# Performance work log

Hardware: AMD Instinct MI355X
Metric: run time of the kernel (lower is better)

## Reference

```python
import jax, jax.numpy as jnp
import numpy as np

N, E, D, H = 20000, 320000, 128, 256
N_ITER = 3

def _w(k, fi, fo):
    return jax.random.normal(k, (fi, fo), jnp.float32) / np.sqrt(fi)

def setup_inputs() -> dict:
    key = jax.random.key(0)
    ks = jax.random.split(key, 16)
    inp = {
        "x": jax.random.normal(ks[0], (N, D), jnp.float32),
        "edge_attr": jax.random.normal(ks[1], (E, D), jnp.float32),
        "edge_index": jax.random.randint(ks[2], (2, E), 0, N, jnp.int32),
        # EASP edge encoder: cat[src,tgt,edge] (3D) -> H -> D
        "enc_w1": _w(ks[3], 3 * D, H), "enc_b1": jnp.zeros((H,), jnp.float32),
        "enc_w2": _w(ks[4], H, D), "enc_b2": jnp.zeros((D,), jnp.float32),
        # EdgeCNN: cat[src(2D), tgt(2D), edge(2D)] = 6D -> H -> D (reattach doubles dims)
        "em_w1": _w(ks[5], 6 * D, H), "em_b1": jnp.zeros((H,), jnp.float32),
        "em_w2": _w(ks[6], H, D), "em_b2": jnp.zeros((D,), jnp.float32),
        # node message MLP: cat[x_src(2D), edge(D)] = 3D -> H -> D
        "nm_w1": _w(ks[7], 3 * D, H), "nm_b1": jnp.zeros((H,), jnp.float32),
        "nm_w2": _w(ks[8], H, D), "nm_b2": jnp.zeros((D,), jnp.float32),
        # node output linear after aggregation
        "no_w": _w(ks[9], D, D), "no_b": jnp.zeros((D,), jnp.float32),
        # shared LayerNorms (ModuleList([layer]*n_iter) shares params)
        "node_ln_g": jnp.ones((D,), jnp.float32), "node_ln_b": jnp.zeros((D,), jnp.float32),
        "edge_ln_g": jnp.ones((D,), jnp.float32), "edge_ln_b": jnp.zeros((D,), jnp.float32),
    }
    return inp

def _ln(v, g, b):
    mu = jnp.mean(v, axis=-1, keepdims=True)
    var = jnp.mean(jnp.square(v - mu), axis=-1, keepdims=True)
    return (v - mu) * jax.lax.rsqrt(var + 1e-5) * g + b

def _mlp2(v, w1, b1, w2, b2):
    return jnp.maximum(v @ w1 + b1, 0.0) @ w2 + b2

def reference(x, edge_attr, edge_index,
              enc_w1, enc_b1, enc_w2, enc_b2,
              em_w1, em_b1, em_w2, em_b2,
              nm_w1, nm_b1, nm_w2, nm_b2,
              no_w, no_b, node_ln_g, node_ln_b, edge_ln_g, edge_ln_b):
    src, tgt = edge_index[0], edge_index[1]
    # edge encoder (EASP)
    init_edge = _mlp2(jnp.concatenate([x[src], x[tgt], edge_attr], axis=1),
                      enc_w1, enc_b1, enc_w2, enc_b2)  # [E, D]
    node_f, edge_f = x, init_edge
    deg = jax.ops.segment_sum(jnp.ones((E,), jnp.float32), tgt, num_segments=N)
    inv_deg = 1.0 / jnp.maximum(deg, 1.0)  # [N]
    for _ in range(N_ITER):
        node_c = jnp.concatenate([x, node_f], axis=1)          # [N, 2D] reattach
        edge_c = jnp.concatenate([init_edge, edge_f], axis=1)  # [E, 2D] reattach
        # edge update
        edge_f = _mlp2(jnp.concatenate([node_c[src], node_c[tgt], edge_c], axis=1),
                       em_w1, em_b1, em_w2, em_b2)             # [E, D]
        # node update: message -> scatter-mean -> linear
        msg = _mlp2(jnp.concatenate([node_c[src], edge_f], axis=1),
                    nm_w1, nm_b1, nm_w2, nm_b2)                # [E, D]
        agg = jax.ops.segment_sum(msg, tgt, num_segments=N) * inv_deg[:, None]
        node_f = agg @ no_w + no_b                             # [N, D]
        # residual + shared LayerNorm
        node_f = _ln(x + node_f, node_ln_g, node_ln_b)
        edge_f = _ln(init_edge + edge_f, edge_ln_g, edge_ln_b)
    return node_f, edge_f
```

## Files before the change

kernel.cpp:

```cpp
#include <hip/hip_runtime.h>
#include <stdint.h>

#define NN 20000
#define NE 320000
#define DD 128
#define HH 256
#define EB 48
#define EBE 64

using ushort8 = __attribute__((ext_vector_type(8))) unsigned short;
using bf16x8  = __attribute__((ext_vector_type(8))) __bf16;
using floatx4 = __attribute__((ext_vector_type(4))) float;

__device__ __forceinline__ unsigned short f2bf(float f) {
  union { float f; uint32_t u; } c; c.f = f;
  uint32_t u = c.u;
  return (unsigned short)((u + 0x7FFFu + ((u >> 16) & 1u)) >> 16);
}
__device__ __forceinline__ float bf2f(unsigned short h) {
  union { uint32_t u; float f; } c; c.u = ((uint32_t)h) << 16;
  return c.f;
}
__device__ __forceinline__ bf16x8 ld_bf8(const unsigned short* p) {
  ushort8 t = *(const ushort8*)p;
  return __builtin_bit_cast(bf16x8, t);
}
__device__ __forceinline__ void split8(const float* p, bf16x8& hi, bf16x8& lo) {
  floatx4 f0 = *(const floatx4*)p;
  floatx4 f1 = *(const floatx4*)(p + 4);
  ushort8 h, l;
#pragma unroll
  for (int k = 0; k < 4; ++k) {
    unsigned short a = f2bf(f0[k]);
    h[k] = a; l[k] = f2bf(f0[k] - bf2f(a));
    unsigned short b = f2bf(f1[k]);
    h[k+4] = b; l[k+4] = f2bf(f1[k] - bf2f(b));
  }
  hi = __builtin_bit_cast(bf16x8, h);
  lo = __builtin_bit_cast(bf16x8, l);
}
__device__ __forceinline__ floatx4 MFMA3(bf16x8 ah, bf16x8 al, bf16x8 bh, bf16x8 bl, floatx4 c) {
  c = __builtin_amdgcn_mfma_f32_16x16x32_bf16(ah, bh, c, 0, 0, 0);
  c = __builtin_amdgcn_mfma_f32_16x16x32_bf16(al, bh, c, 0, 0, 0);
  c = __builtin_amdgcn_mfma_f32_16x16x32_bf16(ah, bl, c, 0, 0, 0);
  return c;
}


__global__ void wconv_kernel(const float* __restrict__ in,
                             unsigned short* __restrict__ out_hi,
                             unsigned short* __restrict__ out_lo,
                             int K, int Nc) {
  int i = blockIdx.x * 256 + threadIdx.x;
  if (i >= K * Nc) return;
  int k = i / Nc, n = i - k * Nc;
  float v = in[i];
  unsigned short h = f2bf(v);
  out_hi[(size_t)n * K + k] = h;
  out_lo[(size_t)n * K + k] = f2bf(v - bf2f(h));
}

__global__ void xconv_kernel(const float* __restrict__ x,
                             unsigned short* __restrict__ xh, unsigned short* __restrict__ xl,
                             unsigned short* __restrict__ nh, unsigned short* __restrict__ nl) {
  int i = blockIdx.x * 256 + threadIdx.x;
  if (i < NN * DD) {
    float v = x[i];
    unsigned short h = f2bf(v), l = f2bf(v - bf2f(h));
    xh[i] = h; xl[i] = l; nh[i] = h; nl[i] = l;
  }
}

__global__ void deg_kernel(const int* __restrict__ ei, float* __restrict__ deg) {
  int e = blockIdx.x * 256 + threadIdx.x;
  if (e < NE) atomicAdd(&deg[ei[NE + e]], 1.0f);
}

__global__ void inv_kernel(const float* __restrict__ deg, float* __restrict__ idg) {
  int n = blockIdx.x * 256 + threadIdx.x;
  if (n < NN) idg[n] = 1.0f / fmaxf(deg[n], 1.0f);
}


template<int NCH, bool USE_NF>
__launch_bounds__(256, 2)
__global__ void nodepre_kernel(
    const unsigned short* __restrict__ xh, const unsigned short* __restrict__ xl,
    const unsigned short* __restrict__ nh, const unsigned short* __restrict__ nl,
    const unsigned short* __restrict__ w0h, const unsigned short* __restrict__ w0l,
    int ko0, int st0, float* __restrict__ out0,
    const unsigned short* __restrict__ w1h, const unsigned short* __restrict__ w1l,
    int ko1, int st1, float* __restrict__ out1,
    const unsigned short* __restrict__ w2h, const unsigned short* __restrict__ w2l,
    int ko2, int st2, float* __restrict__ out2)
{
  const int y = blockIdx.y;
  const unsigned short* Wh = (y == 0) ? w0h : (y == 1) ? w1h : w2h;
  const unsigned short* Wl = (y == 0) ? w0l : (y == 1) ? w1l : w2l;
  const int ko = (y == 0) ? ko0 : (y == 1) ? ko1 : ko2;
  const int st = (y == 0) ? st0 : (y == 1) ? st1 : st2;
  float* out = (y == 0) ? out0 : (y == 1) ? out1 : out2;

  const int tid = threadIdx.x;
  const int n0 = blockIdx.x * 64;
  const int lane = tid & 63, wv = tid >> 6;
  const int lr = lane & 15, kg = lane >> 4;
  int nr[4];
#pragma unroll
  for (int rt = 0; rt < 4; ++rt) {
    const int n = n0 + rt*16 + lr;
    nr[rt] = (n < NN) ? n : (NN - 1);
  }
  const floatx4 Z4 = {0.f, 0.f, 0.f, 0.f};
  floatx4 acc[4][4];
#pragma unroll
  for (int i = 0; i < 4; ++i)
#pragma unroll
    for (int j = 0; j < 4; ++j) acc[i][j] = Z4;

#pragma unroll
  for (int ch = 0; ch < NCH; ++ch) {
    bf16x8 ah[4], al[4], bh[4], bl[4];
#pragma unroll
    for (int rt = 0; rt < 4; ++rt) {
      if (USE_NF && ch >= 4) {
        const size_t off = (size_t)nr[rt] * DD + (ch - 4)*32 + kg*8;
        ah[rt] = ld_bf8(nh + off); al[rt] = ld_bf8(nl + off);
      } else {
        const size_t off = (size_t)nr[rt] * DD + ch*32 + kg*8;
        ah[rt] = ld_bf8(xh + off); al[rt] = ld_bf8(xl + off);
      }
    }
#pragma unroll
    for (int ct = 0; ct < 4; ++ct) {
      const size_t wo = (size_t)(wv*64 + ct*16 + lr) * st + ko + ch*32 + kg*8;
      bh[ct] = ld_bf8(Wh + wo); bl[ct] = ld_bf8(Wl + wo);
    }
#pragma unroll
    for (int rt = 0; rt < 4; ++rt)
#pragma unroll
      for (int ct = 0; ct < 4; ++ct) acc[rt][ct] = MFMA3(ah[rt], al[rt], bh[ct], bl[ct], acc[rt][ct]);
  }
#pragma unroll
  for (int ct = 0; ct < 4; ++ct) {
#pragma unroll
    for (int rt = 0; rt < 4; ++rt)
#pragma unroll
      for (int j = 0; j < 4; ++j) {
        const int n = n0 + rt*16 + kg*4 + j;
        if (n < NN) out[(size_t)n * HH + wv*64 + lr*4 + ct] = acc[rt][ct][j];
      }
  }
}


__launch_bounds__(256, 2)
__global__ void encoder_kernel(
    const float* __restrict__ ea,
    const int* __restrict__ ei,
    const float* __restrict__ pes,
    const float* __restrict__ pet,
    const unsigned short* __restrict__ w1h, const unsigned short* __restrict__ w1l,
    const float* __restrict__ b1,
    const unsigned short* __restrict__ w2h, const unsigned short* __restrict__ w2l,
    const float* __restrict__ b2,
    float* __restrict__ ief32, float* __restrict__ eff32)
{
  __shared__ unsigned short h_hi[EBE * 264];
  __shared__ unsigned short h_lo[EBE * 264];
  __shared__ int sidx[EBE];
  __shared__ int tidx[EBE];
  const int tid = threadIdx.x;
  const int e0 = blockIdx.x * EBE;
  if (tid < EBE) { sidx[tid] = ei[e0 + tid]; tidx[tid] = ei[NE + e0 + tid]; }
  __syncthreads();

  const int lane = tid & 63, wv = tid >> 6;
  const int lr = lane & 15, kg = lane >> 4;
  const floatx4 Z4 = {0.f, 0.f, 0.f, 0.f};

  floatx4 pse[4][4];
#pragma unroll
  for (int rt = 0; rt < 4; ++rt)
#pragma unroll
    for (int j = 0; j < 4; ++j) {
      const int row = rt*16 + kg*4 + j;
      const floatx4 a = *(const floatx4*)(pes + (size_t)sidx[row] * HH + wv*64 + lr*4);
      const floatx4 b = *(const floatx4*)(pet + (size_t)tidx[row] * HH + wv*64 + lr*4);
      pse[rt][j] = a + b;
    }

  floatx4 acc[4][4];
#pragma unroll
  for (int i = 0; i < 4; ++i)
#pragma unroll
    for (int j = 0; j < 4; ++j) acc[i][j] = Z4;
#pragma unroll
  for (int sub = 0; sub < 4; ++sub) {
    const int off = sub*32 + kg*8;
    bf16x8 ah[4], al[4], bh[4], bl[4];
#pragma unroll
    for (int rt = 0; rt < 4; ++rt)
      split8(ea + (size_t)(e0 + rt*16 + lr) * DD + off, ah[rt], al[rt]);
#pragma unroll
    for (int ct = 0; ct < 4; ++ct) {
      const size_t wo = (size_t)(wv*64 + ct*16 + lr) * 384 + 256 + off;
      bh[ct] = ld_bf8(w1h + wo); bl[ct] = ld_bf8(w1l + wo);
    }
#pragma unroll
    for (int rt = 0; rt < 4; ++rt)
#pragma unroll
      for (int ct = 0; ct < 4; ++ct) acc[rt][ct] = MFMA3(ah[rt], al[rt], bh[ct], bl[ct], acc[rt][ct]);
  }
#pragma unroll
  for (int ct = 0; ct < 4; ++ct) {
    const int col = wv*64 + ct*16 + lr;
    const float bias = b1[col];
#pragma unroll
    for (int rt = 0; rt < 4; ++rt)
#pragma unroll
      for (int j = 0; j < 4; ++j) {
        const float v = fmaxf(acc[rt][ct][j] + bias + pse[rt][j][ct], 0.f);
        const unsigned short hh = f2bf(v);
        const int idx = (rt*16 + kg*4 + j) * 264 + col;
        h_hi[idx] = hh;
        h_lo[idx] = f2bf(v - bf2f(hh));
      }
  }
  __syncthreads();

  floatx4 acc2[4][2];
#pragma unroll
  for (int i = 0; i < 4; ++i) { acc2[i][0] = Z4; acc2[i][1] = Z4; }
#pragma unroll
  for (int ch = 0; ch < 8; ++ch) {
    bf16x8 ah[4], al[4], bh[2], bl[2];
#pragma unroll
    for (int rt = 0; rt < 4; ++rt) {
      const int idx = (rt*16 + lr) * 264 + ch*32 + kg*8;
      ah[rt] = ld_bf8(&h_hi[idx]); al[rt] = ld_bf8(&h_lo[idx]);
    }
#pragma unroll
    for (int c2 = 0; c2 < 2; ++c2) {
      const size_t wo = (size_t)(wv*32 + c2*16 + lr) * 256 + ch*32 + kg*8;
      bh[c2] = ld_bf8(w2h + wo); bl[c2] = ld_bf8(w2l + wo);
    }
#pragma unroll
    for (int rt = 0; rt < 4; ++rt)
#pragma unroll
      for (int c2 = 0; c2 < 2; ++c2) acc2[rt][c2] = MFMA3(ah[rt], al[rt], bh[c2], bl[c2], acc2[rt][c2]);
  }
#pragma unroll
  for (int c2 = 0; c2 < 2; ++c2) {
    const int col = wv*32 + c2*16 + lr;
    const float bias = b2[col];
#pragma unroll
    for (int rt = 0; rt < 4; ++rt)
#pragma unroll
      for (int j = 0; j < 4; ++j) {
        const float fv = acc2[rt][c2][j] + bias;
        const size_t idx = (size_t)(e0 + rt*16 + kg*4 + j) * DD + col;
        ief32[idx] = fv;
        eff32[idx] = fv;
      }
  }
}


__launch_bounds__(256, 2)
__global__ void edge_iter_kernel(
    const float* __restrict__ ief32,
    float* __restrict__ eff32,
    const int* __restrict__ ei,
    const float* __restrict__ pse_,
    const float* __restrict__ pte_,
    const float* __restrict__ psm_,
    const unsigned short* __restrict__ ew1h, const unsigned short* __restrict__ ew1l,
    const float* __restrict__ eb1,
    const unsigned short* __restrict__ ew2h, const unsigned short* __restrict__ ew2l,
    const float* __restrict__ eb2,
    const unsigned short* __restrict__ mw1h, const unsigned short* __restrict__ mw1l,
    const float* __restrict__ mb1,
    const unsigned short* __restrict__ mw2h, const unsigned short* __restrict__ mw2l,
    const float* __restrict__ mb2,
    const float* __restrict__ lng, const float* __restrict__ lnb,
    float* __restrict__ agg,
    float* __restrict__ out_edge,
    int write_out)
{
  __shared__ unsigned short h_hi[EB * 264];
  __shared__ unsigned short h_lo[EB * 264];
  __shared__ unsigned short eraw_hi[EB * 136];
  __shared__ unsigned short eraw_lo[EB * 136];
  __shared__ int sidx[EB];
  __shared__ int tidx[EB];

  const int tid = threadIdx.x;
  const int e0 = blockIdx.x * EB;
  if (tid < EB) {
    const int e = e0 + tid;
    const int ec = (e < NE) ? e : (NE - 1);
    sidx[tid] = ei[ec];
    tidx[tid] = ei[NE + ec];
  }
  __syncthreads();

  const int lane = tid & 63, wv = tid >> 6;
  const int lr = lane & 15, kg = lane >> 4;
  int erow_c[3];
#pragma unroll
  for (int rt = 0; rt < 3; ++rt) {
    const int er = e0 + rt*16 + lr;
    erow_c[rt] = (er < NE) ? er : (NE - 1);
  }
  const floatx4 Z4 = {0.f, 0.f, 0.f, 0.f};

  floatx4 pse[3][4];
#pragma unroll
  for (int rt = 0; rt < 3; ++rt)
#pragma unroll
    for (int j = 0; j < 4; ++j) {
      const int row = rt*16 + kg*4 + j;
      const floatx4 a = *(const floatx4*)(pse_ + (size_t)sidx[row] * HH + wv*64 + lr*4);
      const floatx4 b = *(const floatx4*)(pte_ + (size_t)tidx[row] * HH + wv*64 + lr*4);
      pse[rt][j] = a + b;
    }

  floatx4 acc[3][4];
#pragma unroll
  for (int i = 0; i < 3; ++i)
#pragma unroll
    for (int j = 0; j < 4; ++j) acc[i][j] = Z4;

#pragma unroll
  for (int seg = 0; seg < 2; ++seg) {
    const float* fb[3];
#pragma unroll
    for (int rt = 0; rt < 3; ++rt) {
      const size_t e = (size_t)erow_c[rt] * DD;
      fb[rt] = (seg == 0) ? ief32 + e : eff32 + e;
    }
#pragma unroll
    for (int sub = 0; sub < 4; ++sub) {
      const int off = sub*32 + kg*8;
      bf16x8 ah[3], al[3], bh[4], bl[4];
#pragma unroll
      for (int rt = 0; rt < 3; ++rt) split8(fb[rt] + off, ah[rt], al[rt]);
#pragma unroll
      for (int ct = 0; ct < 4; ++ct) {
        const size_t wo = (size_t)(wv*64 + ct*16 + lr) * 768 + 512 + seg*128 + off;
        bh[ct] = ld_bf8(ew1h + wo); bl[ct] = ld_bf8(ew1l + wo);
      }
#pragma unroll
      for (int rt = 0; rt < 3; ++rt)
#pragma unroll
        for (int ct = 0; ct < 4; ++ct) acc[rt][ct] = MFMA3(ah[rt], al[rt], bh[ct], bl[ct], acc[rt][ct]);
    }
  }
#pragma unroll
  for (int ct = 0; ct < 4; ++ct) {
    const int col = wv*64 + ct*16 + lr;
    const float bias = eb1[col];
#pragma unroll
    for (int rt = 0; rt < 3; ++rt)
#pragma unroll
      for (int j = 0; j < 4; ++j) {
        const float v = fmaxf(acc[rt][ct][j] + bias + pse[rt][j][ct], 0.f);
        const unsigned short hh = f2bf(v);
        const int idx = (rt*16 + kg*4 + j) * 264 + col;
        h_hi[idx] = hh;
        h_lo[idx] = f2bf(v - bf2f(hh));
      }
  }
  __syncthreads();

  floatx4 acc2[3][2];
#pragma unroll
  for (int i = 0; i < 3; ++i) { acc2[i][0] = Z4; acc2[i][1] = Z4; }
#pragma unroll
  for (int ch = 0; ch < 8; ++ch) {
    bf16x8 ah[3], al[3], bh[2], bl[2];
#pragma unroll
    for (int rt = 0; rt < 3; ++rt) {
      const int idx = (rt*16 + lr) * 264 + ch*32 + kg*8;
      ah[rt] = ld_bf8(&h_hi[idx]); al[rt] = ld_bf8(&h_lo[idx]);
    }
#pragma unroll
    for (int c2 = 0; c2 < 2; ++c2) {
      const size_t wo = (size_t)(wv*32 + c2*16 + lr) * 256 + ch*32 + kg*8;
      bh[c2] = ld_bf8(ew2h + wo); bl[c2] = ld_bf8(ew2l + wo);
    }
#pragma unroll
    for (int rt = 0; rt < 3; ++rt)
#pragma unroll
      for (int c2 = 0; c2 < 2; ++c2) acc2[rt][c2] = MFMA3(ah[rt], al[rt], bh[c2], bl[c2], acc2[rt][c2]);
  }
#pragma unroll
  for (int c2 = 0; c2 < 2; ++c2) {
    const int col = wv*32 + c2*16 + lr;
    const float bias = eb2[col];
#pragma unroll
    for (int rt = 0; rt < 3; ++rt)
#pragma unroll
      for (int j = 0; j < 4; ++j) {
        const float v = acc2[rt][c2][j] + bias;
        const unsigned short hh = f2bf(v);
        const int idx = (rt*16 + kg*4 + j) * 136 + col;
        eraw_hi[idx] = hh;
        eraw_lo[idx] = f2bf(v - bf2f(hh));
      }
  }
  __syncthreads();

  floatx4 psm[3][4];
#pragma unroll
  for (int rt = 0; rt < 3; ++rt)
#pragma unroll
    for (int j = 0; j < 4; ++j) {
      const int row = rt*16 + kg*4 + j;
      psm[rt][j] = *(const floatx4*)(psm_ + (size_t)sidx[row] * HH + wv*64 + lr*4);
    }

  floatx4 accm[3][4];
#pragma unroll
  for (int i = 0; i < 3; ++i)
#pragma unroll
    for (int j = 0; j < 4; ++j) accm[i][j] = Z4;
#pragma unroll
  for (int sub = 0; sub < 4; ++sub) {
    const int off = sub*32 + kg*8;
    bf16x8 ah[3], al[3], bh[4], bl[4];
#pragma unroll
    for (int rt = 0; rt < 3; ++rt) {
      const int idx = (rt*16 + lr) * 136 + off;
      ah[rt] = ld_bf8(&eraw_hi[idx]); al[rt] = ld_bf8(&eraw_lo[idx]);
    }
#pragma unroll
    for (int ct = 0; ct < 4; ++ct) {
      const size_t wo = (size_t)(wv*64 + ct*16 + lr) * 384 + 256 + off;
      bh[ct] = ld_bf8(mw1h + wo); bl[ct] = ld_bf8(mw1l + wo);
    }
#pragma unroll
    for (int rt = 0; rt < 3; ++rt)
#pragma unroll
      for (int ct = 0; ct < 4; ++ct) accm[rt][ct] = MFMA3(ah[rt], al[rt], bh[ct], bl[ct], accm[rt][ct]);
  }
#pragma unroll
  for (int ct = 0; ct < 4; ++ct) {
    const int col = wv*64 + ct*16 + lr;
    const float bias = mb1[col];
#pragma unroll
    for (int rt = 0; rt < 3; ++rt)
#pragma unroll
      for (int j = 0; j < 4; ++j) {
        const float v = fmaxf(accm[rt][ct][j] + bias + psm[rt][j][ct], 0.f);
        const unsigned short hh = f2bf(v);
        const int idx = (rt*16 + kg*4 + j) * 264 + col;
        h_hi[idx] = hh;
        h_lo[idx] = f2bf(v - bf2f(hh));
      }
  }
  __syncthreads();

  floatx4 accq[3][2];
#pragma unroll
  for (int i = 0; i < 3; ++i) { accq[i][0] = Z4; accq[i][1] = Z4; }
#pragma unroll
  for (int ch = 0; ch < 8; ++ch) {
    bf16x8 ah[3], al[3], bh[2], bl[2];
#pragma unroll
    for (int rt = 0; rt < 3; ++rt) {
      const int idx = (rt*16 + lr) * 264 + ch*32 + kg*8;
      ah[rt] = ld_bf8(&h_hi[idx]); al[rt] = ld_bf8(&h_lo[idx]);
    }
#pragma unroll
    for (int c2 = 0; c2 < 2; ++c2) {
      const size_t wo = (size_t)(wv*32 + c2*16 + lr) * 256 + ch*32 + kg*8;
      bh[c2] = ld_bf8(mw2h + wo); bl[c2] = ld_bf8(mw2l + wo);
    }
#pragma unroll
    for (int rt = 0; rt < 3; ++rt)
#pragma unroll
      for (int c2 = 0; c2 < 2; ++c2) accq[rt][c2] = MFMA3(ah[rt], al[rt], bh[c2], bl[c2], accq[rt][c2]);
  }
#pragma unroll
  for (int c2 = 0; c2 < 2; ++c2) {
    const int col = wv*32 + c2*16 + lr;
    const float bias = mb2[col];
#pragma unroll
    for (int rt = 0; rt < 3; ++rt)
#pragma unroll
      for (int j = 0; j < 4; ++j) {
        const int row = rt*16 + kg*4 + j;
        if (e0 + row < NE)
          atomicAdd(&agg[(size_t)tidx[row] * DD + col], accq[rt][c2][j] + bias);
      }
  }

  if (tid < EB * 4) {
    const int row = tid >> 2, sub = tid & 3;
    const int er = e0 + row;
    if (er < NE) {
      const size_t e = (size_t)er;
      float v[32];
      float s = 0.f, ss = 0.f;
#pragma unroll
      for (int c8 = 0; c8 < 4; ++c8) {
        const int li = row * 136 + sub*32 + c8*8;
        ushort8 rh = *(const ushort8*)&eraw_hi[li];
        ushort8 rl = *(const ushort8*)&eraw_lo[li];
        const float* ip = &ief32[e * DD + sub*32 + c8*8];
        floatx4 i0 = *(const floatx4*)ip;
        floatx4 i1 = *(const floatx4*)(ip + 4);
#pragma unroll
        for (int k = 0; k < 4; ++k) {
          float v0 = (bf2f(rh[k]) + bf2f(rl[k])) + i0[k];
          float v1 = (bf2f(rh[k+4]) + bf2f(rl[k+4])) + i1[k];
          v[c8*8 + k] = v0; v[c8*8 + 4 + k] = v1;
          s += v0 + v1; ss += v0*v0 + v1*v1;
        }
      }
      s  += __shfl_xor(s, 1);  s  += __shfl_xor(s, 2);
      ss += __shfl_xor(ss, 1); ss += __shfl_xor(ss, 2);
      const float mu  = s * (1.f/128.f);
      const float var = ss * (1.f/128.f) - mu * mu;
      const float inv = rsqrtf(fmaxf(var, 0.f) + 1e-5f);
#pragma unroll
      for (int c8 = 0; c8 < 4; ++c8) {
        floatx4 o0, o1;
#pragma unroll
        for (int k = 0; k < 8; ++k) {
          const int col = sub*32 + c8*8 + k;
          const float o = (v[c8*8 + k] - mu) * inv * lng[col] + lnb[col];
          if (k < 4) o0[k] = o; else o1[k-4] = o;
        }
        *(floatx4*)&eff32[e * DD + sub*32 + c8*8] = o0;
        *(floatx4*)&eff32[e * DD + sub*32 + c8*8 + 4] = o1;
        if (write_out) {
          *(floatx4*)&out_edge[e * DD + sub*32 + c8*8] = o0;
          *(floatx4*)&out_edge[e * DD + sub*32 + c8*8 + 4] = o1;
        }
      }
    }
  }
}


__launch_bounds__(256, 2)
__global__ void node_update_kernel(
    const float* __restrict__ agg, const float* __restrict__ idg,
    const unsigned short* __restrict__ nwh, const unsigned short* __restrict__ nwl,
    const float* __restrict__ nb,
    const float* __restrict__ x,
    const float* __restrict__ lng, const float* __restrict__ lnb,
    float* __restrict__ out_node,
    unsigned short* __restrict__ nh, unsigned short* __restrict__ nl,
    int write_out)
{
  __shared__ unsigned short a_hi[64 * 136];
  __shared__ unsigned short a_lo[64 * 136];
  __shared__ float o_lds[64 * 132];
  const int tid = threadIdx.x;
  const int n0 = blockIdx.x * 64;
  const int row = tid >> 2, sub = tid & 3;
  const int n = n0 + row;
  {
    const float s = (n < NN) ? idg[n] : 0.f;
#pragma unroll
    for (int c4 = 0; c4 < 8; ++c4) {
      floatx4 v = {0.f, 0.f, 0.f, 0.f};
      if (n < NN) v = *(const floatx4*)&agg[(size_t)n * DD + sub*32 + c4*4];
#pragma unroll
      for (int k = 0; k < 4; ++k) {
        const float f = v[k] * s;
        const unsigned short hh = f2bf(f);
        const int idx = row * 136 + sub*32 + c4*4 + k;
        a_hi[idx] = hh;
        a_lo[idx] = f2bf(f - bf2f(hh));
      }
    }
  }
  __syncthreads();

  const int lane = tid & 63, wv = tid >> 6;
  const int lr = lane & 15, kg = lane >> 4;
  const floatx4 Z4 = {0.f, 0.f, 0.f, 0.f};
  floatx4 acc[4][2];
#pragma unroll
  for (int i = 0; i < 4; ++i) { acc[i][0] = Z4; acc[i][1] = Z4; }
#pragma unroll
  for (int ch = 0; ch < 4; ++ch) {
    bf16x8 ah[4], al[4], bh[2], bl[2];
#pragma unroll
    for (int rt = 0; rt < 4; ++rt) {
      const int idx = (rt*16 + lr) * 136 + ch*32 + kg*8;
      ah[rt] = ld_bf8(&a_hi[idx]); al[rt] = ld_bf8(&a_lo[idx]);
    }
#pragma unroll
    for (int c2 = 0; c2 < 2; ++c2) {
      const size_t wo = (size_t)(wv*32 + c2*16 + lr) * DD + ch*32 + kg*8;
      bh[c2] = ld_bf8(nwh + wo); bl[c2] = ld_bf8(nwl + wo);
    }
#pragma unroll
    for (int rt = 0; rt < 4; ++rt)
#pragma unroll
      for (int c2 = 0; c2 < 2; ++c2) acc[rt][c2] = MFMA3(ah[rt], al[rt], bh[c2], bl[c2], acc[rt][c2]);
  }
#pragma unroll
  for (int c2 = 0; c2 < 2; ++c2) {
    const int col = wv*32 + c2*16 + lr;
    const float bias = nb[col];
#pragma unroll
    for (int rt = 0; rt < 4; ++rt)
#pragma unroll
      for (int j = 0; j < 4; ++j)
        o_lds[(rt*16 + kg*4 + j) * 132 + col] = acc[rt][c2][j] + bias;
  }
  __syncthreads();

  if (n < NN) {
    float v[32];
    float s = 0.f, ss = 0.f;
#pragma unroll
    for (int c4 = 0; c4 < 8; ++c4) {
      floatx4 xa = *(const floatx4*)&x[(size_t)n * DD + sub*32 + c4*4];
#pragma unroll
      for (int k = 0; k < 4; ++k) {
        const float val = o_lds[row * 132 + sub*32 + c4*4 + k] + xa[k];
        v[c4*4 + k] = val; s += val; ss += val * val;
      }
    }
    s  += __shfl_xor(s, 1);  s  += __shfl_xor(s, 2);
    ss += __shfl_xor(ss, 1); ss += __shfl_xor(ss, 2);
    const float mu  = s * (1.f/128.f);
    const float var = ss * (1.f/128.f) - mu * mu;
    const float inv = rsqrtf(fmaxf(var, 0.f) + 1e-5f);
#pragma unroll
    for (int c8 = 0; c8 < 4; ++c8) {
      floatx4 o0, o1; ushort8 oh, ol;
#pragma unroll
      for (int k = 0; k < 8; ++k) {
        const int col = sub*32 + c8*8 + k;
        const float o = (v[c8*8 + k] - mu) * inv * lng[col] + lnb[col];
        if (k < 4) o0[k] = o; else o1[k-4] = o;
        const unsigned short hh = f2bf(o);
        oh[k] = hh;
        ol[k] = f2bf(o - bf2f(hh));
      }
      if (write_out) {
        *(floatx4*)&out_node[(size_t)n * DD + sub*32 + c8*8] = o0;
        *(floatx4*)&out_node[(size_t)n * DD + sub*32 + c8*8 + 4] = o1;
      }
      *(ushort8*)&nh[(size_t)n * DD + sub*32 + c8*8] = oh;
      *(ushort8*)&nl[(size_t)n * DD + sub*32 + c8*8] = ol;
    }
  }
}


extern "C" void kernel_launch(void* const* d_in, const int* in_sizes, int n_in,
                              void* d_out, int out_size, void* d_ws, size_t ws_size,
                              hipStream_t stream) {
  (void)in_sizes; (void)n_in; (void)out_size; (void)ws_size;

  const float* x      = (const float*)d_in[0];
  const float* ea     = (const float*)d_in[1];
  const int*   ei     = (const int*)d_in[2];
  const float* enc_w1 = (const float*)d_in[3];
  const float* enc_b1 = (const float*)d_in[4];
  const float* enc_w2 = (const float*)d_in[5];
  const float* enc_b2 = (const float*)d_in[6];
  const float* em_w1  = (const float*)d_in[7];
  const float* em_b1  = (const float*)d_in[8];
  const float* em_w2  = (const float*)d_in[9];
  const float* em_b2  = (const float*)d_in[10];
  const float* nm_w1  = (const float*)d_in[11];
  const float* nm_b1  = (const float*)d_in[12];
  const float* nm_w2  = (const float*)d_in[13];
  const float* nm_b2  = (const float*)d_in[14];
  const float* no_w   = (const float*)d_in[15];
  const float* no_b   = (const float*)d_in[16];
  const float* nlng   = (const float*)d_in[17];
  const float* nlnb   = (const float*)d_in[18];
  const float* elng   = (const float*)d_in[19];
  const float* elnb   = (const float*)d_in[20];

  float* out_node = (float*)d_out;
  float* ief32    = out_node + (size_t)NN * DD;

  char* p = (char*)d_ws;
  auto alloc = [&](size_t bytes) -> void* {
    void* r = (void*)p;
    p += (bytes + 255) & ~(size_t)255;
    return r;
  };
  unsigned short* xb_h = (unsigned short*)alloc((size_t)NN * DD * 2);
  unsigned short* xb_l = (unsigned short*)alloc((size_t)NN * DD * 2);
  unsigned short* nf_h = (unsigned short*)alloc((size_t)NN * DD * 2);
  unsigned short* nf_l = (unsigned short*)alloc((size_t)NN * DD * 2);
  float*          eff32 = (float*)alloc((size_t)NE * DD * 4);
  float*          agg  = (float*)alloc((size_t)NN * DD * 4);
  float*          deg  = (float*)alloc((size_t)NN * 4);
  float*          idg  = (float*)alloc((size_t)NN * 4);
  float*          psrc_e = (float*)alloc((size_t)NN * HH * 4);
  float*          ptgt_e = (float*)alloc((size_t)NN * HH * 4);
  float*          psrc_m = (float*)alloc((size_t)NN * HH * 4);
  unsigned short* cw1h = (unsigned short*)alloc((size_t)384 * 256 * 2);
  unsigned short* cw1l = (unsigned short*)alloc((size_t)384 * 256 * 2);
  unsigned short* cw2h = (unsigned short*)alloc((size_t)256 * 128 * 2);
  unsigned short* cw2l = (unsigned short*)alloc((size_t)256 * 128 * 2);
  unsigned short* ew1h = (unsigned short*)alloc((size_t)768 * 256 * 2);
  unsigned short* ew1l = (unsigned short*)alloc((size_t)768 * 256 * 2);
  unsigned short* ew2h = (unsigned short*)alloc((size_t)256 * 128 * 2);
  unsigned short* ew2l = (unsigned short*)alloc((size_t)256 * 128 * 2);
  unsigned short* mw1h = (unsigned short*)alloc((size_t)384 * 256 * 2);
  unsigned short* mw1l = (unsigned short*)alloc((size_t)384 * 256 * 2);
  unsigned short* mw2h = (unsigned short*)alloc((size_t)256 * 128 * 2);
  unsigned short* mw2l = (unsigned short*)alloc((size_t)256 * 128 * 2);
  unsigned short* nwh  = (unsigned short*)alloc((size_t)128 * 128 * 2);
  unsigned short* nwl  = (unsigned short*)alloc((size_t)128 * 128 * 2);

  wconv_kernel<<<(384*256 + 255)/256, 256, 0, stream>>>(enc_w1, cw1h, cw1l, 384, 256);
  wconv_kernel<<<(256*128 + 255)/256, 256, 0, stream>>>(enc_w2, cw2h, cw2l, 256, 128);
  wconv_kernel<<<(768*256 + 255)/256, 256, 0, stream>>>(em_w1, ew1h, ew1l, 768, 256);
  wconv_kernel<<<(256*128 + 255)/256, 256, 0, stream>>>(em_w2, ew2h, ew2l, 256, 128);
  wconv_kernel<<<(384*256 + 255)/256, 256, 0, stream>>>(nm_w1, mw1h, mw1l, 384, 256);
  wconv_kernel<<<(256*128 + 255)/256, 256, 0, stream>>>(nm_w2, mw2h, mw2l, 256, 128);
  wconv_kernel<<<(128*128 + 255)/256, 256, 0, stream>>>(no_w, nwh, nwl, 128, 128);

  xconv_kernel<<<(NN*DD + 255)/256, 256, 0, stream>>>(x, xb_h, xb_l, nf_h, nf_l);

  hipMemsetAsync(deg, 0, (size_t)NN * 4, stream);
  deg_kernel<<<(NE + 255)/256, 256, 0, stream>>>(ei, deg);
  inv_kernel<<<(NN + 255)/256, 256, 0, stream>>>(deg, idg);

  nodepre_kernel<4, false><<<dim3(313, 2), 256, 0, stream>>>(
      xb_h, xb_l, nf_h, nf_l,
      cw1h, cw1l, 0,   384, psrc_e,
      cw1h, cw1l, 128, 384, ptgt_e,
      cw1h, cw1l, 0,   384, psrc_e);

  encoder_kernel<<<NE/EBE, 256, 0, stream>>>(ea, ei, psrc_e, ptgt_e,
                                             cw1h, cw1l, enc_b1, cw2h, cw2l, enc_b2,
                                             ief32, eff32);

  const int egrid = (NE + EB - 1) / EB;
  for (int it = 0; it < 3; ++it) {
    const int last = (it == 2) ? 1 : 0;
    nodepre_kernel<8, true><<<dim3(313, 3), 256, 0, stream>>>(
        xb_h, xb_l, nf_h, nf_l,
        ew1h, ew1l, 0,   768, psrc_e,
        ew1h, ew1l, 256, 768, ptgt_e,
        mw1h, mw1l, 0,   384, psrc_m);
    hipMemsetAsync(agg, 0, (size_t)NN * DD * 4, stream);
    edge_iter_kernel<<<egrid, 256, 0, stream>>>(
        ief32, eff32, ei, psrc_e, ptgt_e, psrc_m,
        ew1h, ew1l, em_b1, ew2h, ew2l, em_b2,
        mw1h, mw1l, nm_b1, mw2h, mw2l, nm_b2,
        elng, elnb, agg, ief32, last);
    node_update_kernel<<<(NN + 63)/64, 256, 0, stream>>>(
        agg, idg, nwh, nwl, no_b, x, nlng, nlnb, out_node, nf_h, nf_l, last);
  }
}
```

Measured before the change: 3.450 ms.

## Raise edge tile to 64 rows and alias LDS buffers in edge kernel

The edge block grows from 48 to 64 edges, so each wave handles four row tiles and every weight fragment loaded from global memory feeds more MFMAs. The separate eraw buffers are folded into one shared hi/lo buffer, and the edge LayerNorm moves ahead of the second message MLP so the buffer can be reused. Because 64 divides the edge count, the tail clamping and bounds checks are removed. In exchange the kernel needs more accumulator registers, which may lower occupancy, and it adds an extra barrier.

```diff
diff --git a/kernel.cpp b/kernel.cpp
--- a/kernel.cpp
+++ b/kernel.cpp
@@ -5,7 +5,7 @@
 #define NE 320000
 #define DD 128
 #define HH 256
-#define EB 48
+#define EB 64
 #define EBE 64
 
 using ushort8 = __attribute__((ext_vector_type(8))) unsigned short;
@@ -288,36 +288,26 @@
     float* __restrict__ out_edge,
     int write_out)
 {
-  __shared__ unsigned short h_hi[EB * 264];
-  __shared__ unsigned short h_lo[EB * 264];
-  __shared__ unsigned short eraw_hi[EB * 136];
-  __shared__ unsigned short eraw_lo[EB * 136];
+  __shared__ unsigned short bufh[EB * 264];
+  __shared__ unsigned short bufl[EB * 264];
   __shared__ int sidx[EB];
   __shared__ int tidx[EB];
 
   const int tid = threadIdx.x;
   const int e0 = blockIdx.x * EB;
   if (tid < EB) {
-    const int e = e0 + tid;
-    const int ec = (e < NE) ? e : (NE - 1);
-    sidx[tid] = ei[ec];
-    tidx[tid] = ei[NE + ec];
+    sidx[tid] = ei[e0 + tid];
+    tidx[tid] = ei[NE + e0 + tid];
   }
   __syncthreads();
 
   const int lane = tid & 63, wv = tid >> 6;
   const int lr = lane & 15, kg = lane >> 4;
-  int erow_c[3];
-#pragma unroll
-  for (int rt = 0; rt < 3; ++rt) {
-    const int er = e0 + rt*16 + lr;
-    erow_c[rt] = (er < NE) ? er : (NE - 1);
-  }
   const floatx4 Z4 = {0.f, 0.f, 0.f, 0.f};
 
-  floatx4 pse[3][4];
-#pragma unroll
-  for (int rt = 0; rt < 3; ++rt)
+  floatx4 pse[4][4];
+#pragma unroll
+  for (int rt = 0; rt < 4; ++rt)
 #pragma unroll
     for (int j = 0; j < 4; ++j) {
       const int row = rt*16 + kg*4 + j;
@@ -326,33 +316,33 @@
       pse[rt][j] = a + b;
     }
 
-  floatx4 acc[3][4];
-#pragma unroll
-  for (int i = 0; i < 3; ++i)
+  floatx4 acc[4][4];
+#pragma unroll
+  for (int i = 0; i < 4; ++i)
 #pragma unroll
     for (int j = 0; j < 4; ++j) acc[i][j] = Z4;
 
 #pragma unroll
   for (int seg = 0; seg < 2; ++seg) {
-    const float* fb[3];
-#pragma unroll
-    for (int rt = 0; rt < 3; ++rt) {
-      const size_t e = (size_t)erow_c[rt] * DD;
+    const float* fb[4];
+#pragma unroll
+    for (int rt = 0; rt < 4; ++rt) {
+      const size_t e = (size_t)(e0 + rt*16 + lr) * DD;
       fb[rt] = (seg == 0) ? ief32 + e : eff32 + e;
     }
 #pragma unroll
     for (int sub = 0; sub < 4; ++sub) {
       const int off = sub*32 + kg*8;
-      bf16x8 ah[3], al[3], bh[4], bl[4];
-#pragma unroll
-      for (int rt = 0; rt < 3; ++rt) split8(fb[rt] + off, ah[rt], al[rt]);
+      bf16x8 ah[4], al[4], bh[4], bl[4];
+#pragma unroll
+      for (int rt = 0; rt < 4; ++rt) split8(fb[rt] + off, ah[rt], al[rt]);
 #pragma unroll
       for (int ct = 0; ct < 4; ++ct) {
         const size_t wo = (size_t)(wv*64 + ct*16 + lr) * 768 + 512 + seg*128 + off;
         bh[ct] = ld_bf8(ew1h + wo); bl[ct] = ld_bf8(ew1l + wo);
       }
 #pragma unroll
-      for (int rt = 0; rt < 3; ++rt)
+      for (int rt = 0; rt < 4; ++rt)
 #pragma unroll
         for (int ct = 0; ct < 4; ++ct) acc[rt][ct] = MFMA3(ah[rt], al[rt], bh[ct], bl[ct], acc[rt][ct]);
     }
@@ -362,28 +352,28 @@
     const int col = wv*64 + ct*16 + lr;
     const float bias = eb1[col];
 #pragma unroll
-    for (int rt = 0; rt < 3; ++rt)
+    for (int rt = 0; rt < 4; ++rt)
 #pragma unroll
       for (int j = 0; j < 4; ++j) {
         const float v = fmaxf(acc[rt][ct][j] + bias + pse[rt][j][ct], 0.f);
         const unsigned short hh = f2bf(v);
         const int idx = (rt*16 + kg*4 + j) * 264 + col;
-        h_hi[idx] = hh;
-        h_lo[idx] = f2bf(v - bf2f(hh));
-      }
-  }
-  __syncthreads();
-
-  floatx4 acc2[3][2];
-#pragma unroll
-  for (int i = 0; i < 3; ++i) { acc2[i][0] = Z4; acc2[i][1] = Z4; }
+        bufh[idx] = hh;
+        bufl[idx] = f2bf(v - bf2f(hh));
+      }
+  }
+  __syncthreads();
+
+  floatx4 acc2[4][2];
+#pragma unroll
+  for (int i = 0; i < 4; ++i) { acc2[i][0] = Z4; acc2[i][1] = Z4; }
 #pragma unroll
   for (int ch = 0; ch < 8; ++ch) {
-    bf16x8 ah[3], al[3], bh[2], bl[2];
-#pragma unroll
-    for (int rt = 0; rt < 3; ++rt) {
+    bf16x8 ah[4], al[4], bh[2], bl[2];
+#pragma unroll
+    for (int rt = 0; rt < 4; ++rt) {
       const int idx = (rt*16 + lr) * 264 + ch*32 + kg*8;
-      ah[rt] = ld_bf8(&h_hi[idx]); al[rt] = ld_bf8(&h_lo[idx]);
+      ah[rt] = ld_bf8(&bufh[idx]); al[rt] = ld_bf8(&bufl[idx]);
     }
 #pragma unroll
     for (int c2 = 0; c2 < 2; ++c2) {
@@ -391,49 +381,51 @@
       bh[c2] = ld_bf8(ew2h + wo); bl[c2] = ld_bf8(ew2l + wo);
     }
 #pragma unroll
-    for (int rt = 0; rt < 3; ++rt)
+    for (int rt = 0; rt < 4; ++rt)
 #pragma unroll
       for (int c2 = 0; c2 < 2; ++c2) acc2[rt][c2] = MFMA3(ah[rt], al[rt], bh[c2], bl[c2], acc2[rt][c2]);
   }
+  __syncthreads();
+
 #pragma unroll
   for (int c2 = 0; c2 < 2; ++c2) {
     const int col = wv*32 + c2*16 + lr;
     const float bias = eb2[col];
 #pragma unroll
-    for (int rt = 0; rt < 3; ++rt)
+    for (int rt = 0; rt < 4; ++rt)
 #pragma unroll
       for (int j = 0; j < 4; ++j) {
         const float v = acc2[rt][c2][j] + bias;
         const unsigned short hh = f2bf(v);
         const int idx = (rt*16 + kg*4 + j) * 136 + col;
-        eraw_hi[idx] = hh;
-        eraw_lo[idx] = f2bf(v - bf2f(hh));
-      }
-  }
-  __syncthreads();
-
-  floatx4 psm[3][4];
-#pragma unroll
-  for (int rt = 0; rt < 3; ++rt)
+        bufh[idx] = hh;
+        bufl[idx] = f2bf(v - bf2f(hh));
+      }
+  }
+  __syncthreads();
+
+  floatx4 psm[4][4];
+#pragma unroll
+  for (int rt = 0; rt < 4; ++rt)
 #pragma unroll
     for (int j = 0; j < 4; ++j) {
       const int row = rt*16 + kg*4 + j;
       psm[rt][j] = *(const floatx4*)(psm_ + (size_t)sidx[row] * HH + wv*64 + lr*4);
     }
 
-  floatx4 accm[3][4];
-#pragma unroll
-  for (int i = 0; i < 3; ++i)
+  floatx4 accm[4][4];
+#pragma unroll
+  for (int i = 0; i < 4; ++i)
 #pragma unroll
     for (int j = 0; j < 4; ++j) accm[i][j] = Z4;
 #pragma unroll
   for (int sub = 0; sub < 4; ++sub) {
     const int off = sub*32 + kg*8;
-    bf16x8 ah[3], al[3], bh[4], bl[4];
-#pragma unroll
-    for (int rt = 0; rt < 3; ++rt) {
+    bf16x8 ah[4], al[4], bh[4], bl[4];
+#pragma unroll
+    for (int rt = 0; rt < 4; ++rt) {
       const int idx = (rt*16 + lr) * 136 + off;
-      ah[rt] = ld_bf8(&eraw_hi[idx]); al[rt] = ld_bf8(&eraw_lo[idx]);
+      ah[rt] = ld_bf8(&bufh[idx]); al[rt] = ld_bf8(&bufl[idx]);
     }
 #pragma unroll
     for (int ct = 0; ct < 4; ++ct) {
@@ -441,37 +433,83 @@
       bh[ct] = ld_bf8(mw1h + wo); bl[ct] = ld_bf8(mw1l + wo);
     }
 #pragma unroll
-    for (int rt = 0; rt < 3; ++rt)
+    for (int rt = 0; rt < 4; ++rt)
 #pragma unroll
       for (int ct = 0; ct < 4; ++ct) accm[rt][ct] = MFMA3(ah[rt], al[rt], bh[ct], bl[ct], accm[rt][ct]);
   }
+
+  {
+    const int row = tid >> 2, sub = tid & 3;
+    const size_t e = (size_t)(e0 + row);
+    float v[32];
+    float s = 0.f, ss = 0.f;
+#pragma unroll
+    for (int c8 = 0; c8 < 4; ++c8) {
+      const int li = row * 136 + sub*32 + c8*8;
+      ushort8 rh = *(const ushort8*)&bufh[li];
+      ushort8 rl = *(const ushort8*)&bufl[li];
+      const float* ip = &ief32[e * DD + sub*32 + c8*8];
+      floatx4 i0 = *(const floatx4*)ip;
+      floatx4 i1 = *(const floatx4*)(ip + 4);
+#pragma unroll
+      for (int k = 0; k < 4; ++k) {
+        float v0 = (bf2f(rh[k]) + bf2f(rl[k])) + i0[k];
+        float v1 = (bf2f(rh[k+4]) + bf2f(rl[k+4])) + i1[k];
+        v[c8*8 + k] = v0; v[c8*8 + 4 + k] = v1;
+        s += v0 + v1; ss += v0*v0 + v1*v1;
+      }
+    }
+    s  += __shfl_xor(s, 1);  s  += __shfl_xor(s, 2);
+    ss += __shfl_xor(ss, 1); ss += __shfl_xor(ss, 2);
+    const float mu  = s * (1.f/128.f);
+    const float var = ss * (1.f/128.f) - mu * mu;
+    const float inv = rsqrtf(fmaxf(var, 0.f) + 1e-5f);
+#pragma unroll
+    for (int c8 = 0; c8 < 4; ++c8) {
+      floatx4 o0, o1;
+#pragma unroll
+      for (int k = 0; k < 8; ++k) {
+        const int col = sub*32 + c8*8 + k;
+        const float o = (v[c8*8 + k] - mu) * inv * lng[col] + lnb[col];
+        if (k < 4) o0[k] = o; else o1[k-4] = o;
+      }
+      *(floatx4*)&eff32[e * DD + sub*32 + c8*8] = o0;
+      *(floatx4*)&eff32[e * DD + sub*32 + c8*8 + 4] = o1;
+      if (write_out) {
+        *(floatx4*)&out_edge[e * DD + sub*32 + c8*8] = o0;
+        *(floatx4*)&out_edge[e * DD + sub*32 + c8*8 + 4] = o1;
+      }
+    }
+  }
+  __syncthreads();
+
 #pragma unroll
   for (int ct = 0; ct < 4; ++ct) {
     const int col = wv*64 + ct*16 + lr;
     const float bias = mb1[col];
 #pragma unroll
-    for (int rt = 0; rt < 3; ++rt)
+    for (int rt = 0; rt < 4; ++rt)
 #pragma unroll
       for (int j = 0; j < 4; ++j) {
         const float v = fmaxf(accm[rt][ct][j] + bias + psm[rt][j][ct], 0.f);
         const unsigned short hh = f2bf(v);
         const int idx = (rt*16 + kg*4 + j) * 264 + col;
-        h_hi[idx] = hh;
-        h_lo[idx] = f2bf(v - bf2f(hh));
-      }
-  }
-  __syncthreads();
-
-  floatx4 accq[3][2];
-#pragma unroll
-  for (int i = 0; i < 3; ++i) { accq[i][0] = Z4; accq[i][1] = Z4; }
+        bufh[idx] = hh;
+        bufl[idx] = f2bf(v - bf2f(hh));
+      }
+  }
+  __syncthreads();
+
+  floatx4 accq[4][2];
+#pragma unroll
+  for (int i = 0; i < 4; ++i) { accq[i][0] = Z4; accq[i][1] = Z4; }
 #pragma unroll
   for (int ch = 0; ch < 8; ++ch) {
-    bf16x8 ah[3], al[3], bh[2], bl[2];
-#pragma unroll
-    for (int rt = 0; rt < 3; ++rt) {
+    bf16x8 ah[4], al[4], bh[2], bl[2];
+#pragma unroll
+    for (int rt = 0; rt < 4; ++rt) {
       const int idx = (rt*16 + lr) * 264 + ch*32 + kg*8;
-      ah[rt] = ld_bf8(&h_hi[idx]); al[rt] = ld_bf8(&h_lo[idx]);
+      ah[rt] = ld_bf8(&bufh[idx]); al[rt] = ld_bf8(&bufl[idx]);
     }
 #pragma unroll
     for (int c2 = 0; c2 < 2; ++c2) {
@@ -479,7 +517,7 @@
       bh[c2] = ld_bf8(mw2h + wo); bl[c2] = ld_bf8(mw2l + wo);
     }
 #pragma unroll
-    for (int rt = 0; rt < 3; ++rt)
+    for (int rt = 0; rt < 4; ++rt)
 #pragma unroll
       for (int c2 = 0; c2 < 2; ++c2) accq[rt][c2] = MFMA3(ah[rt], al[rt], bh[c2], bl[c2], accq[rt][c2]);
   }
@@ -488,60 +526,12 @@
     const int col = wv*32 + c2*16 + lr;
     const float bias = mb2[col];
 #pragma unroll
-    for (int rt = 0; rt < 3; ++rt)
+    for (int rt = 0; rt < 4; ++rt)
 #pragma unroll
       for (int j = 0; j < 4; ++j) {
         const int row = rt*16 + kg*4 + j;
-        if (e0 + row < NE)
-          atomicAdd(&agg[(size_t)tidx[row] * DD + col], accq[rt][c2][j] + bias);
-      }
-  }
-
-  if (tid < EB * 4) {
-    const int row = tid >> 2, sub = tid & 3;
-    const int er = e0 + row;
-    if (er < NE) {
-      const size_t e = (size_t)er;
-      float v[32];
-      float s = 0.f, ss = 0.f;
-#pragma unroll
-      for (int c8 = 0; c8 < 4; ++c8) {
-        const int li = row * 136 + sub*32 + c8*8;
-        ushort8 rh = *(const ushort8*)&eraw_hi[li];
-        ushort8 rl = *(const ushort8*)&eraw_lo[li];
-        const float* ip = &ief32[e * DD + sub*32 + c8*8];
-        floatx4 i0 = *(const floatx4*)ip;
-        floatx4 i1 = *(const floatx4*)(ip + 4);
-#pragma unroll
-        for (int k = 0; k < 4; ++k) {
-          float v0 = (bf2f(rh[k]) + bf2f(rl[k])) + i0[k];
-          float v1 = (bf2f(rh[k+4]) + bf2f(rl[k+4])) + i1[k];
-          v[c8*8 + k] = v0; v[c8*8 + 4 + k] = v1;
-          s += v0 + v1; ss += v0*v0 + v1*v1;
-        }
-      }
-      s  += __shfl_xor(s, 1);  s  += __shfl_xor(s, 2);
-      ss += __shfl_xor(ss, 1); ss += __shfl_xor(ss, 2);
-      const float mu  = s * (1.f/128.f);
-      const float var = ss * (1.f/128.f) - mu * mu;
-      const float inv = rsqrtf(fmaxf(var, 0.f) + 1e-5f);
-#pragma unroll
-      for (int c8 = 0; c8 < 4; ++c8) {
-        floatx4 o0, o1;
-#pragma unroll
-        for (int k = 0; k < 8; ++k) {
-          const int col = sub*32 + c8*8 + k;
-          const float o = (v[c8*8 + k] - mu) * inv * lng[col] + lnb[col];
-          if (k < 4) o0[k] = o; else o1[k-4] = o;
-        }
-        *(floatx4*)&eff32[e * DD + sub*32 + c8*8] = o0;
-        *(floatx4*)&eff32[e * DD + sub*32 + c8*8 + 4] = o1;
-        if (write_out) {
-          *(floatx4*)&out_edge[e * DD + sub*32 + c8*8] = o0;
-          *(floatx4*)&out_edge[e * DD + sub*32 + c8*8 + 4] = o1;
-        }
-      }
-    }
+        atomicAdd(&agg[(size_t)tidx[row] * DD + col], accq[rt][c2][j] + bias);
+      }
   }
 }
 
@@ -744,7 +734,7 @@
                                              cw1h, cw1l, enc_b1, cw2h, cw2l, enc_b2,
                                              ief32, eff32);
 
-  const int egrid = (NE + EB - 1) / EB;
+  const int egrid = NE / EB;
   for (int it = 0; it < 3; ++it) {
     const int last = (it == 2) ? 1 : 0;
     nodepre_kernel<8, true><<<dim3(313, 3), 256, 0, stream>>>(
```

Result: faster. 3.198 ms (-7.3%).
